# Optimization experiments

Hardware: AMD Instinct MI355X
Metric: run time of the kernel (lower is better)

Reference implementation:

```python
import jax, jax.numpy as jnp
import numpy as np

C = 256
BN_EPS = 1e-5


def conv1x1(x, w, b):
    # x: (B, Cin, H, W), w: (Cout, Cin), b: (Cout,)
    return jnp.einsum('bchw,oc->bohw', x, w) + b[None, :, None, None]


def setup_inputs() -> dict:
    key = jax.random.key(0)
    ks = jax.random.split(key, 12)
    B, H, W = 8, 64, 64
    s = 1.0 / np.sqrt(C)
    inp = {
        'xi': jax.random.normal(ks[0], (B, C, H, W), jnp.float32),
        'xj': jax.random.normal(ks[1], (B, C, H, W), jnp.float32),
        'g_w': jax.random.normal(ks[2], (C, C), jnp.float32) * s,
        'g_b': jax.random.normal(ks[3], (C,), jnp.float32) * s,
        'theta_w': jax.random.normal(ks[4], (C, C), jnp.float32) * s,
        'theta_b': jax.random.normal(ks[5], (C,), jnp.float32) * s,
        'phi_w': jax.random.normal(ks[6], (C, C), jnp.float32) * s,
        'phi_b': jax.random.normal(ks[7], (C,), jnp.float32) * s,
        'W_w': jax.random.normal(ks[8], (C, C), jnp.float32) * s,
        'W_b': jax.random.normal(ks[9], (C,), jnp.float32) * s,
        'bn_gamma': jnp.ones((C,), jnp.float32),
        'bn_beta': jnp.zeros((C,), jnp.float32),
    }
    return inp


def reference(xi, xj, g_w, g_b, theta_w, theta_b, phi_w, phi_b, W_w, W_b, bn_gamma, bn_beta):
    B, Cc, H, W = xi.shape
    N = H * W
    # 1x1 conv projections, flattened to token sequences
    g_x = conv1x1(xj, g_w, g_b).reshape(B, Cc, N)        # (B, C, N)
    theta_x = conv1x1(xi, theta_w, theta_b).reshape(B, Cc, N)  # (B, C, N)
    phi_x = conv1x1(xj, phi_w, phi_b).reshape(B, Cc, N)  # (B, C, N)
    # f = theta^T @ phi, scaled by N (no softmax)
    f = jnp.einsum('bcn,bcm->bnm', theta_x, phi_x) / N   # (B, N, N)
    # y = f @ g^T, back to channel-first
    y = jnp.einsum('bnm,bcm->bcn', f, g_x).reshape(B, Cc, H, W)
    W_y = conv1x1(y, W_w, W_b)
    z = W_y + xi
    # BatchNorm2d (training-mode batch statistics, biased variance)
    mean = jnp.mean(z, axis=(0, 2, 3), keepdims=True)
    var = jnp.var(z, axis=(0, 2, 3), keepdims=True)
    z_hat = (z - mean) * jax.lax.rsqrt(var + BN_EPS)
    return z_hat * bn_gamma[None, :, None, None] + bn_beta[None, :, None, None]
```

## Files before the change

### kernel.cpp

```cpp
#include <hip/hip_runtime.h>
#include <hip/hip_cooperative_groups.h>
#include <cstddef>

namespace cg = cooperative_groups;

#define CCH 256
#define NPIX 4096
#define NB 8
#define INVCNT (1.0f/32768.0f)
#define INVN (1.0f/4096.0f)

typedef __bf16 bf16_t;
typedef __attribute__((ext_vector_type(8))) __bf16 bf16x8;
typedef __attribute__((ext_vector_type(4))) __bf16 bf16x4;
typedef __attribute__((ext_vector_type(4))) float f32x4;

#define OFF_S      0u
#define OFF_AB     2048u
#define OFF_BMT    34816u
#define OFF_T1     67584u
#define OFF_R      67840u
#define OFF_W1     68096u
#define OFF_C1     68352u
#define OFF_G      68608u
#define OFF_MP     330752u
#define OFF_E      592896u
#define OFF_RSP    594944u
#define OFF_BSUM   627712u
#define OFF_BSQ    627968u
#define OFF_GP     890368u
#define OFF_XIT    5084672u

__device__ __forceinline__ void pack8(const float4& x, const float4& y, bf16x8& o) {
  o[0]=(bf16_t)x.x; o[1]=(bf16_t)x.y; o[2]=(bf16_t)x.z; o[3]=(bf16_t)x.w;
  o[4]=(bf16_t)y.x; o[5]=(bf16_t)y.y; o[6]=(bf16_t)y.z; o[7]=(bf16_t)y.w;
}

__device__ __forceinline__ void ld4(const float* p, float4& a0, float4& a1, float4& a2, float4& a3) {
  a0 = *(const float4*)p;       a1 = *(const float4*)(p + 4);
  a2 = *(const float4*)(p + 8); a3 = *(const float4*)(p + 12);
}

template <bool ATRANS>
__device__ __forceinline__ void mm64v(const float* __restrict__ A,
                                      const float* __restrict__ B,
                                      int i0, int j0,
                                      float (&acc)[2][4],
                                      float (*s1)[65], float (*s2)[65]) {
  const int t = threadIdx.x, tx = t & 15, ty = t >> 4;
  for (int k0 = 0; k0 < 256; k0 += 64) {
#pragma unroll
    for (int it = 0; it < 2; ++it) {
      const int f = t + 512 * it;
      const int row = f >> 4, cc = (f & 15) * 4;
      float4 va;
      if (ATRANS)
        va = *(const float4*)(A + (size_t)(k0 + row) * CCH + i0 + cc);
      else
        va = *(const float4*)(A + (size_t)(i0 + row) * CCH + k0 + cc);
      const float4 vb = *(const float4*)(B + (size_t)(k0 + row) * CCH + j0 + cc);
      s1[row][cc + 0] = va.x; s1[row][cc + 1] = va.y; s1[row][cc + 2] = va.z; s1[row][cc + 3] = va.w;
      s2[row][cc + 0] = vb.x; s2[row][cc + 1] = vb.y; s2[row][cc + 2] = vb.z; s2[row][cc + 3] = vb.w;
    }
    __syncthreads();
#pragma unroll 4
    for (int kk = 0; kk < 64; ++kk) {
      float ar[2], br[4];
#pragma unroll
      for (int i = 0; i < 2; ++i) ar[i] = ATRANS ? s1[kk][2 * ty + i] : s1[2 * ty + i][kk];
#pragma unroll
      for (int j = 0; j < 4; ++j) br[j] = s2[kk][4 * tx + j];
#pragma unroll
      for (int i = 0; i < 2; ++i)
#pragma unroll
        for (int j = 0; j < 4; ++j) acc[i][j] += ar[i] * br[j];
    }
    __syncthreads();
  }
}

__device__ void pre_body(int blk, const float* Ww, const float* gw, const float* phw,
                         const float* thw, const float* gb, const float* phb,
                         const float* thb, float* ws, unsigned char* SMEM) {
  const int t = threadIdx.x;
  if (blk < 32) {
    float (*s1)[65] = (float(*)[65])SMEM;
    float (*s2)[65] = (float(*)[65])(SMEM + 16640);
    const int tb = blk & 15;
    const int i0 = (tb >> 2) * 64, j0 = (tb & 3) * 64;
    float acc[2][4] = {};
    if (blk < 16) mm64v<false>(Ww, gw, i0, j0, acc, s1, s2);
    else          mm64v<true >(thw, phw, i0, j0, acc, s1, s2);
    bf16_t* outp = (bf16_t*)(ws + (blk < 16 ? OFF_AB : OFF_BMT));
    const int tx = t & 15, ty = t >> 4;
#pragma unroll
    for (int i = 0; i < 2; ++i) {
      bf16x4 mv;
#pragma unroll
      for (int q = 0; q < 4; ++q) mv[q] = (bf16_t)acc[i][q];
      *(bf16x4*)&outp[(size_t)(i0 + 2 * ty + i) * CCH + j0 + 4 * tx] = mv;
    }
  } else {
    if (t < 256) {
      float t1v = 0.f, rv = 0.f, w1v = 0.f;
      for (int k = 0; k < 256; ++k) {
        t1v += phw[k * CCH + t] * thb[k];
        rv  += thw[k * CCH + t] * phb[k];
        w1v += Ww[t * CCH + k] * gb[k];
      }
      ws[OFF_T1 + t] = t1v; ws[OFF_R + t] = rv; ws[OFF_W1 + t] = w1v;
    }
    float* red = (float*)SMEM;
    red[t] = (t < 256) ? phb[t] * thb[t] : 0.f;
    __syncthreads();
    for (int off = 256; off; off >>= 1) { if (t < off) red[t] += red[t + off]; __syncthreads(); }
    if (t == 0) ws[OFF_C1] = red[0];
  }
}

__device__ void cvtT_body(int bx, int b, const float* __restrict__ xi,
                          float* __restrict__ ws, unsigned char* SMEM) {
  bf16_t (*st)[72] = (bf16_t(*)[72])SMEM;
  const int c0 = (bx & 1) * 128;
  const int n0 = (bx >> 1) * 64;
  const float* X = xi + (size_t)b * CCH * NPIX;
  const int t = threadIdx.x;
  const int r = t >> 2, c4 = (t & 3) * 16;
  {
    float4 a0, a1, a2, a3;
    ld4(X + (size_t)(c0 + r) * NPIX + n0 + c4, a0, a1, a2, a3);
    bf16x8 u0, u1;
    pack8(a0, a1, u0); pack8(a2, a3, u1);
    *(bf16x8*)&st[r][c4] = u0;
    *(bf16x8*)&st[r][c4 + 8] = u1;
  }
  __syncthreads();
  bf16_t* Xit = (bf16_t*)(ws + OFF_XIT) + (size_t)b * NPIX * CCH;
  const int nr = t >> 3, cc = (t & 7) * 16;
  bf16x8 o0, o1;
#pragma unroll
  for (int j = 0; j < 8; ++j) o0[j] = st[cc + j][nr];
#pragma unroll
  for (int j = 0; j < 8; ++j) o1[j] = st[cc + 8 + j][nr];
  *(bf16x8*)(Xit + (size_t)(n0 + nr) * CCH + c0 + cc) = o0;
  *(bf16x8*)(Xit + (size_t)(n0 + nr) * CCH + c0 + cc + 8) = o1;
}

__device__ void gram_body(int ks, int b, const float* __restrict__ X,
                          float* __restrict__ ws, unsigned char* SMEM) {
  bf16_t (*sA)[256][40] = (bf16_t(*)[256][40])SMEM;
  const int t = threadIdx.x;
  const int w = t >> 6, lane = t & 63;
  const int wr = w >> 1, wc = w & 1;
  const int lr = lane & 15, hi = lane >> 4;
  const int fcol = 8 * hi;
  const f32x4 z4 = {0.f, 0.f, 0.f, 0.f};
  f32x4 acc[4][8];
#pragma unroll
  for (int fr = 0; fr < 4; ++fr)
#pragma unroll
    for (int fc = 0; fc < 8; ++fc) acc[fr][fc] = z4;
  float rsum = 0.f;
  const int k0 = ks * 256;
  const int srow = t >> 1, sh16 = (t & 1) * 16;

  float4 a0, a1, a2, a3;
  auto LOAD = [&](int kc) {
    ld4(X + (size_t)srow * NPIX + k0 + kc + sh16, a0, a1, a2, a3);
    rsum += a0.x + a0.y + a0.z + a0.w + a1.x + a1.y + a1.z + a1.w
          + a2.x + a2.y + a2.z + a2.w + a3.x + a3.y + a3.z + a3.w;
  };
  auto WRITE = [&](int q) {
    bf16x8 u0, u1;
    pack8(a0, a1, u0); pack8(a2, a3, u1);
    *(bf16x8*)&sA[q][srow][sh16] = u0;
    *(bf16x8*)&sA[q][srow][sh16 + 8] = u1;
  };

  LOAD(0);
  WRITE(0);
  __syncthreads();
  int cur = 0;
  for (int kc8 = 0; kc8 < 8; ++kc8) {
    if (kc8 < 7) LOAD(32 * (kc8 + 1));
    bf16x8 af[4];
#pragma unroll
    for (int fr = 0; fr < 4; ++fr)
      af[fr] = *(const bf16x8*)&sA[cur][64 * wr + 16 * fr + lr][fcol];
#pragma unroll
    for (int fc = 0; fc < 8; ++fc) {
      const bf16x8 bv = *(const bf16x8*)&sA[cur][128 * wc + 16 * fc + lr][fcol];
#pragma unroll
      for (int fr = 0; fr < 4; ++fr)
        acc[fr][fc] = __builtin_amdgcn_mfma_f32_16x16x32_bf16(af[fr], bv, acc[fr][fc], 0, 0, 0);
    }
    if (kc8 < 7) WRITE(cur ^ 1);
    __syncthreads();
    cur ^= 1;
  }

  {
    const float o = __shfl_down(rsum, 1);
    if (!(t & 1)) ws[OFF_RSP + ((size_t)(b * 16 + ks)) * CCH + srow] = rsum + o;
  }
  bf16_t* GPp = (bf16_t*)(ws + OFF_GP) + (size_t)(b * 16 + ks) * 65536;
  bf16_t (*sT)[264] = (bf16_t(*)[264])SMEM;
  const int rl = 16 * wr + 4 * hi;
#pragma unroll
  for (int fr = 0; fr < 4; ++fr) {
    __syncthreads();
#pragma unroll
    for (int fc = 0; fc < 8; ++fc)
#pragma unroll
      for (int reg = 0; reg < 4; ++reg)
        sT[rl + reg][128 * wc + 16 * fc + lr] = (bf16_t)acc[fr][fc][reg];
    __syncthreads();
    const int row = t >> 3;
    const int c32 = (t & 7) * 32;
    const int grow = 64 * (row >> 4) + 16 * fr + (row & 15);
#pragma unroll
    for (int q = 0; q < 4; ++q) {
      const bf16x8 v = *(const bf16x8*)&sT[row][c32 + 8 * q];
      *(bf16x8*)&GPp[(size_t)grow * CCH + c32 + 8 * q] = v;
    }
  }
}

__global__ __launch_bounds__(512) void k_mega(const float* __restrict__ xi,
                                              const float* __restrict__ xj,
                                              const float* __restrict__ Ww,
                                              const float* __restrict__ gw,
                                              const float* __restrict__ phw,
                                              const float* __restrict__ thw,
                                              const float* __restrict__ gb,
                                              const float* __restrict__ phb,
                                              const float* __restrict__ thb,
                                              float* __restrict__ ws) {
  __shared__ __align__(16) unsigned char SMEM[40960];
  const int bx = blockIdx.x, by = blockIdx.y;
  if (bx >= 144) {
    if (by == 0) pre_body(bx - 144, Ww, gw, phw, thw, gb, phb, thb, ws, SMEM);
    return;
  }
  if (bx >= 16) { cvtT_body(bx - 16, by, xi, ws, SMEM); return; }
  gram_body(bx, by, xj + (size_t)by * CCH * NPIX, ws, SMEM);
}

__global__ __launch_bounds__(256) void k_greduce(float* __restrict__ ws) {
  const int b = blockIdx.y, bx = blockIdx.x, t = threadIdx.x;
  const bf16_t* GPp = (const bf16_t*)(ws + OFF_GP) + (size_t)b * 16 * 65536;
  bf16_t* Gb = (bf16_t*)(ws + OFF_G) + (size_t)b * 65536;
  const int row = bx * 8 + (t >> 5);
  const int j8 = (t & 31) * 8;
  float s[8] = {};
#pragma unroll
  for (int ks = 0; ks < 16; ++ks) {
    const bf16x8 v = *(const bf16x8*)&GPp[(size_t)ks * 65536 + row * CCH + j8];
#pragma unroll
    for (int q = 0; q < 8; ++q) s[q] += (float)v[q];
  }
  bf16x8 o;
#pragma unroll
  for (int q = 0; q < 8; ++q) o[q] = (bf16_t)s[q];
  *(bf16x8*)&Gb[(size_t)row * CCH + j8] = o;
  if (t < 128) {
    const int rr = bx * 8 + (t >> 4), l = t & 15;
    float v = ws[OFF_RSP + ((size_t)(b * 16 + l)) * CCH + rr];
#pragma unroll
    for (int off = 8; off; off >>= 1) v += __shfl_down(v, off, 16);
    if (l == 0) ws[OFF_S + b * CCH + rr] = v;
  }
}

__global__ __launch_bounds__(256) void k_kmmat(const float* __restrict__ Wb, float* __restrict__ ws) {
  const int b = blockIdx.y;
  const int i0 = blockIdx.x * 32;
  const int t = threadIdx.x;
  const int w = t >> 6, lane = t & 63;
  const int rg = w >> 1, cw = w & 1;
  const int lr = lane & 15, hi = lane >> 4;
  const int fcol = 8 * hi;

  __shared__ __align__(16) bf16_t sA[2][32][40];
  __shared__ __align__(16) bf16_t sB[2][256][40];
  __shared__ __align__(16) bf16_t sK[32][264];
  __shared__ float sS[256], sT1[256], sR[256], sW1[256], sVS[256];
  __shared__ float sU[32];
  __shared__ float red[256];
  __shared__ float sdt_sh;

  const bf16_t* Ab  = (const bf16_t*)(ws + OFF_AB);
  const bf16_t* BmT = (const bf16_t*)(ws + OFF_BMT);
  const bf16_t* Gb  = (const bf16_t*)(ws + OFF_G) + (size_t)b * 65536;

  sS[t]  = ws[OFF_S + b * CCH + t];
  sT1[t] = ws[OFF_T1 + t];
  sR[t]  = ws[OFF_R + t];
  sW1[t] = ws[OFF_W1 + t];
  __syncthreads();
  red[t] = sS[t] * sT1[t];
  __syncthreads();
  for (int off = 128; off; off >>= 1) { if (t < off) red[t] += red[t + off]; __syncthreads(); }
  if (t == 0) sdt_sh = red[0];
  {
    float a = 0.f;
    for (int k8 = 0; k8 < 256; k8 += 8) {
      const bf16x8 v = *(const bf16x8*)&BmT[(size_t)t * CCH + k8];
#pragma unroll
      for (int q = 0; q < 8; ++q) a += (float)v[q] * sS[k8 + q];
    }
    sVS[t] = a;
  }
  if (t < 32) {
    float a = 0.f;
    for (int k8 = 0; k8 < 256; k8 += 8) {
      const bf16x8 v = *(const bf16x8*)&Ab[(size_t)(i0 + t) * CCH + k8];
#pragma unroll
      for (int q = 0; q < 8; ++q) a += (float)v[q] * sS[k8 + q];
    }
    sU[t] = a;
  }

  const f32x4 z4 = {0.f, 0.f, 0.f, 0.f};
  const int arow = t >> 2, achk = (t & 3) * 8;

  f32x4 acc[8];
#pragma unroll
  for (int fc = 0; fc < 8; ++fc) acc[fc] = z4;
  bf16x8 ra;
  bf16x8 gb8[4];
  auto LOADB = [&](int k) {
    if (t < 128) ra = *(const bf16x8*)&Ab[(size_t)(i0 + arow) * CCH + k + achk];
#pragma unroll
    for (int h = 0; h < 4; ++h)
      gb8[h] = *(const bf16x8*)&Gb[(size_t)(64 * h + arow) * CCH + k + achk];
  };
  auto WRITEB = [&](int q) {
    if (t < 128) *(bf16x8*)&sA[q][arow][achk] = ra;
#pragma unroll
    for (int h = 0; h < 4; ++h)
      *(bf16x8*)&sB[q][64 * h + arow][achk] = gb8[h];
  };
  LOADB(0);
  WRITEB(0);
  __syncthreads();
  int cur = 0;
  for (int ks = 0; ks < 8; ++ks) {
    if (ks < 7) LOADB(32 * (ks + 1));
    const bf16x8 af = *(const bf16x8*)&sA[cur][16 * rg + lr][fcol];
#pragma unroll
    for (int fc = 0; fc < 8; ++fc) {
      const bf16x8 bv = *(const bf16x8*)&sB[cur][128 * cw + 16 * fc + lr][fcol];
      acc[fc] = __builtin_amdgcn_mfma_f32_16x16x32_bf16(af, bv, acc[fc], 0, 0, 0);
    }
    if (ks < 7) WRITEB(cur ^ 1);
    __syncthreads();
    cur ^= 1;
  }
#pragma unroll
  for (int fc = 0; fc < 8; ++fc)
#pragma unroll
    for (int reg = 0; reg < 4; ++reg)
      sK[16 * rg + 4 * hi + reg][128 * cw + 16 * fc + lr] = (bf16_t)acc[fc][reg];
  __syncthreads();

  if (t < 32) {
    float dot = 0.f;
    for (int k8 = 0; k8 < 256; k8 += 8) {
      const bf16x8 v = *(const bf16x8*)&sK[t][k8];
#pragma unroll
      for (int q = 0; q < 8; ++q) dot += (float)v[q] * sT1[k8 + q];
    }
    const float c1 = ws[OFF_C1];
    const float ui = sU[t], w1i = sW1[i0 + t];
    ws[OFF_E + b * CCH + i0 + t] = INVN * (dot + c1 * ui + sdt_sh * w1i) + c1 * w1i + Wb[i0 + t];
  }

  f32x4 acc2[8];
#pragma unroll
  for (int fc = 0; fc < 8; ++fc) acc2[fc] = z4;
  bf16x8 rb[4];
  auto LOADC = [&](int k) {
#pragma unroll
    for (int h = 0; h < 4; ++h)
      rb[h] = *(const bf16x8*)&BmT[(size_t)(64 * h + arow) * CCH + k + achk];
  };
  auto WRITEC = [&](int q) {
#pragma unroll
    for (int h = 0; h < 4; ++h)
      *(bf16x8*)&sB[q][64 * h + arow][achk] = rb[h];
  };
  LOADC(0);
  WRITEC(0);
  __syncthreads();
  cur = 0;
  for (int ks = 0; ks < 8; ++ks) {
    if (ks < 7) LOADC(32 * (ks + 1));
    const bf16x8 af = *(const bf16x8*)&sK[16 * rg + lr][32 * ks + fcol];
#pragma unroll
    for (int fc = 0; fc < 8; ++fc) {
      const bf16x8 bv = *(const bf16x8*)&sB[cur][128 * cw + 16 * fc + lr][fcol];
      acc2[fc] = __builtin_amdgcn_mfma_f32_16x16x32_bf16(af, bv, acc2[fc], 0, 0, 0);
    }
    if (ks < 7) WRITEC(cur ^ 1);
    __syncthreads();
    cur ^= 1;
  }

  bf16_t* Mp = (bf16_t*)(ws + OFF_MP) + (size_t)b * 65536;
#pragma unroll
  for (int fc = 0; fc < 8; ++fc) {
    const int j = 128 * cw + 16 * fc + lr;
    const float rj = sR[j], vsj = sVS[j];
#pragma unroll
    for (int reg = 0; reg < 4; ++reg) {
      const int il = 16 * rg + 4 * hi + reg;
      const float ui = sU[il], w1i = sW1[i0 + il];
      float m = (acc2[fc][reg] + ui * rj + w1i * vsj) * INVN + w1i * rj;
      if (i0 + il == j) m += 1.0f;
      sK[16 * rg + 4 * hi + reg][128 * cw + 16 * fc + lr] = (bf16_t)m;
    }
  }
  __syncthreads();
  {
    const int row = t >> 3;
    const int c32 = (t & 7) * 32;
#pragma unroll
    for (int q = 0; q < 4; ++q) {
      const bf16x8 v = *(const bf16x8*)&sK[row][c32 + 8 * q];
      *(bf16x8*)&Mp[(size_t)(i0 + row) * CCH + c32 + 8 * q] = v;
    }
  }
}

__device__ __forceinline__ void zmm_core(const float* __restrict__ ws, int b, int n0,
                                         f32x4 (&acc)[2][8],
                                         bf16_t (*sA)[64][40], bf16_t (*sB)[256][40]) {
  const int t = threadIdx.x;
  const int lane = t & 63;
  const int w = t >> 6;
  const int rg = w >> 1, cw = w & 1;
  const int lr = lane & 15, hi = lane >> 4;
  const bf16_t* Xit = (const bf16_t*)(ws + OFF_XIT) + (size_t)b * NPIX * CCH;
  const bf16_t* Mp = (const bf16_t*)(ws + OFF_MP) + (size_t)b * 65536;
  const int arow = t >> 2, achk = (t & 3) * 8;
  bf16x8 ra, rb0, rb1, rb2, rb3;
  ra  = *(const bf16x8*)(Xit + (size_t)(n0 + arow) * CCH + achk);
  rb0 = *(const bf16x8*)(Mp + (size_t)(arow)       * CCH + achk);
  rb1 = *(const bf16x8*)(Mp + (size_t)(64 + arow)  * CCH + achk);
  rb2 = *(const bf16x8*)(Mp + (size_t)(128 + arow) * CCH + achk);
  rb3 = *(const bf16x8*)(Mp + (size_t)(192 + arow) * CCH + achk);
  *(bf16x8*)&sA[0][arow][achk] = ra;
  *(bf16x8*)&sB[0][arow][achk] = rb0;
  *(bf16x8*)&sB[0][64 + arow][achk] = rb1;
  *(bf16x8*)&sB[0][128 + arow][achk] = rb2;
  *(bf16x8*)&sB[0][192 + arow][achk] = rb3;
  __syncthreads();
  int cur = 0;
  for (int ks = 0; ks < 8; ++ks) {
    const int nk = 32 * (ks + 1);
    if (ks < 7) {
      ra  = *(const bf16x8*)(Xit + (size_t)(n0 + arow) * CCH + nk + achk);
      rb0 = *(const bf16x8*)(Mp + (size_t)(arow)       * CCH + nk + achk);
      rb1 = *(const bf16x8*)(Mp + (size_t)(64 + arow)  * CCH + nk + achk);
      rb2 = *(const bf16x8*)(Mp + (size_t)(128 + arow) * CCH + nk + achk);
      rb3 = *(const bf16x8*)(Mp + (size_t)(192 + arow) * CCH + nk + achk);
    }
    const int fcol = 8 * hi;
    const bf16x8 af0 = *(const bf16x8*)&sA[cur][32 * rg + lr][fcol];
    const bf16x8 af1 = *(const bf16x8*)&sA[cur][32 * rg + 16 + lr][fcol];
#pragma unroll
    for (int fc = 0; fc < 8; ++fc) {
      const bf16x8 bv = *(const bf16x8*)&sB[cur][128 * cw + 16 * fc + lr][fcol];
      acc[0][fc] = __builtin_amdgcn_mfma_f32_16x16x32_bf16(af0, bv, acc[0][fc], 0, 0, 0);
      acc[1][fc] = __builtin_amdgcn_mfma_f32_16x16x32_bf16(af1, bv, acc[1][fc], 0, 0, 0);
    }
    if (ks < 7) {
      *(bf16x8*)&sA[cur ^ 1][arow][achk] = ra;
      *(bf16x8*)&sB[cur ^ 1][arow][achk] = rb0;
      *(bf16x8*)&sB[cur ^ 1][64 + arow][achk] = rb1;
      *(bf16x8*)&sB[cur ^ 1][128 + arow][achk] = rb2;
      *(bf16x8*)&sB[cur ^ 1][192 + arow][achk] = rb3;
    }
    __syncthreads();
    cur ^= 1;
  }
}

__device__ __forceinline__ void bn_partials_atomic(float* __restrict__ ws, const float* sE,
                                                   f32x4 (&acc)[2][8],
                                                   float (*redS)[128], float (*redQ)[128]) {
  const int t = threadIdx.x;
  const int lane = t & 63, w = t >> 6;
  const int cw = w & 1, lr = lane & 15;
  float ps[8], pq[8];
#pragma unroll
  for (int fc = 0; fc < 8; ++fc) {
    const int c = 128 * cw + 16 * fc + lr;
    const float e = sE[c];
    float s = 0.f, q = 0.f;
#pragma unroll
    for (int fr = 0; fr < 2; ++fr)
#pragma unroll
      for (int reg = 0; reg < 4; ++reg) {
        const float z = acc[fr][fc][reg] + e;
        s += z; q += z * z;
      }
    s += __shfl_xor(s, 16); s += __shfl_xor(s, 32);
    q += __shfl_xor(q, 16); q += __shfl_xor(q, 32);
    ps[fc] = s; pq[fc] = q;
  }
  if (lane < 16) {
#pragma unroll
    for (int fc = 0; fc < 8; ++fc) {
      redS[w][16 * fc + lane] = ps[fc];
      redQ[w][16 * fc + lane] = pq[fc];
    }
  }
  __syncthreads();
  {
    const int cg2 = t >> 7, c = t & 127;
    float s = 0.f, q = 0.f;
#pragma unroll
    for (int rg2 = 0; rg2 < 2; ++rg2) {
      s += redS[rg2 * 2 + cg2][c];
      q += redQ[rg2 * 2 + cg2][c];
    }
    atomicAdd(&ws[OFF_BSUM + t], s);
    atomicAdd(&ws[OFF_BSQ + t], q);
  }
}

__device__ __forceinline__ void z_apply(const float* sC1, const float* sC2,
                                        f32x4 (&acc)[2][8],
                                        float* __restrict__ out, int b, int n0) {
  const int t = threadIdx.x;
  const int lane = t & 63, w = t >> 6;
  const int rg = w >> 1, cw = w & 1;
  const int lr = lane & 15, hi = lane >> 4;
#pragma unroll
  for (int fc = 0; fc < 8; ++fc) {
    const int c = 128 * cw + 16 * fc + lr;
    const float sc = sC1[c], b2 = sC2[c];
    float* op = out + ((size_t)b * CCH + c) * NPIX + n0 + 32 * rg + 4 * hi;
#pragma unroll
    for (int fr = 0; fr < 2; ++fr) {
      float4 v;
      v.x = acc[fr][fc][0] * sc + b2;
      v.y = acc[fr][fc][1] * sc + b2;
      v.z = acc[fr][fc][2] * sc + b2;
      v.w = acc[fr][fc][3] * sc + b2;
      *(float4*)(op + 16 * fr) = v;
    }
  }
}

__global__ __launch_bounds__(256) void k_zstat(float* __restrict__ ws) {
  const int b = blockIdx.y, n0 = blockIdx.x * 64;
  const int t = threadIdx.x;
  __shared__ __align__(16) bf16_t sA[2][64][40];
  __shared__ __align__(16) bf16_t sB[2][256][40];
  __shared__ float sE[256];
  __shared__ float redS[4][128], redQ[4][128];
  sE[t] = ws[OFF_E + b * CCH + t];
  const f32x4 z4 = {0.f, 0.f, 0.f, 0.f};
  f32x4 acc[2][8];
#pragma unroll
  for (int fr = 0; fr < 2; ++fr)
#pragma unroll
    for (int fc = 0; fc < 8; ++fc) acc[fr][fc] = z4;
  zmm_core(ws, b, n0, acc, sA, sB);
  bn_partials_atomic(ws, sE, acc, redS, redQ);
}

__global__ __launch_bounds__(256) void k_zapply(float* __restrict__ ws, float* __restrict__ out,
                                                const float* __restrict__ gamma,
                                                const float* __restrict__ beta) {
  const int b = blockIdx.y, n0 = blockIdx.x * 64;
  const int t = threadIdx.x;
  __shared__ __align__(16) bf16_t sA[2][64][40];
  __shared__ __align__(16) bf16_t sB[2][256][40];
  __shared__ float sC1[256], sC2[256];
  {
    const float e = ws[OFF_E + b * CCH + t];
    const float sv = ws[OFF_BSUM + t], qv = ws[OFF_BSQ + t];
    const float mean = sv * INVCNT;
    const float var = qv * INVCNT - mean * mean;
    const float sc = gamma[t] * rsqrtf(var + 1e-5f);
    sC1[t] = sc;
    sC2[t] = e * sc + beta[t] - mean * sc;
  }
  const f32x4 z4 = {0.f, 0.f, 0.f, 0.f};
  f32x4 acc[2][8];
#pragma unroll
  for (int fr = 0; fr < 2; ++fr)
#pragma unroll
    for (int fc = 0; fc < 8; ++fc) acc[fr][fc] = z4;
  zmm_core(ws, b, n0, acc, sA, sB);
  z_apply(sC1, sC2, acc, out, b, n0);
}

__global__ __launch_bounds__(256, 2) void k_zfused(float* __restrict__ ws,
                                                   float* __restrict__ out,
                                                   const float* __restrict__ gamma,
                                                   const float* __restrict__ beta) {
  const int bid = blockIdx.x;
  const int b = bid >> 6, n0 = (bid & 63) * 64;
  const int t = threadIdx.x;
  __shared__ __align__(16) bf16_t sA[2][64][40];
  __shared__ __align__(16) bf16_t sB[2][256][40];
  __shared__ float sE[256];
  __shared__ float sC1[256], sC2[256];
  __shared__ float redS[4][128], redQ[4][128];
  sE[t] = ws[OFF_E + b * CCH + t];
  const f32x4 z4 = {0.f, 0.f, 0.f, 0.f};
  f32x4 acc[2][8];
#pragma unroll
  for (int fr = 0; fr < 2; ++fr)
#pragma unroll
    for (int fc = 0; fc < 8; ++fc) acc[fr][fc] = z4;
  zmm_core(ws, b, n0, acc, sA, sB);
  bn_partials_atomic(ws, sE, acc, redS, redQ);
  cg::this_grid().sync();
  {
    const float sv = ws[OFF_BSUM + t], qv = ws[OFF_BSQ + t];
    const float mean = sv * INVCNT;
    const float var = qv * INVCNT - mean * mean;
    const float sc = gamma[t] * rsqrtf(var + 1e-5f);
    sC1[t] = sc;
    sC2[t] = sE[t] * sc + beta[t] - mean * sc;
  }
  __syncthreads();
  z_apply(sC1, sC2, acc, out, b, n0);
}

extern "C" void kernel_launch(void* const* d_in, const int* in_sizes, int n_in,
                              void* d_out, int out_size, void* d_ws, size_t ws_size,
                              hipStream_t stream) {
  const float* xi  = (const float*)d_in[0];
  const float* xj  = (const float*)d_in[1];
  const float* gw  = (const float*)d_in[2];
  const float* gb  = (const float*)d_in[3];
  const float* thw = (const float*)d_in[4];
  const float* thb = (const float*)d_in[5];
  const float* phw = (const float*)d_in[6];
  const float* phb = (const float*)d_in[7];
  const float* Ww  = (const float*)d_in[8];
  const float* Wb  = (const float*)d_in[9];
  const float* gamma = (const float*)d_in[10];
  const float* beta  = (const float*)d_in[11];
  float* ws = (float*)d_ws;
  float* out = (float*)d_out;

  k_mega<<<dim3(177, 8), 512, 0, stream>>>(xi, xj, Ww, gw, phw, thw, gb, phb, thb, ws);
  k_greduce<<<dim3(32, 8), 256, 0, stream>>>(ws);
  k_kmmat<<<dim3(8, 8), 256, 0, stream>>>(Wb, ws);
  hipMemsetAsync(ws + OFF_BSUM, 0, 512 * sizeof(float), stream);

  int dev = 0;
  hipGetDevice(&dev);
  int coopAttr = 0;
  hipDeviceGetAttribute(&coopAttr, hipDeviceAttributeCooperativeLaunch, dev);
  int maxb = 0;
  if (coopAttr)
    hipOccupancyMaxActiveBlocksPerMultiprocessor(&maxb, k_zfused, 256, 0);

  bool done = false;
  if (coopAttr && maxb >= 2) {
    float* wsp = ws;
    float* outp = out;
    const float* gammap = gamma;
    const float* betap = beta;
    void* args[] = {(void*)&wsp, (void*)&outp, (void*)&gammap, (void*)&betap};
    hipError_t err = hipLaunchCooperativeKernel((void*)k_zfused, dim3(512), dim3(256),
                                                args, 0, stream);
    done = (err == hipSuccess);
  }
  if (!done) {
    k_zstat<<<dim3(64, 8), 256, 0, stream>>>(ws);
    k_zapply<<<dim3(64, 8), 256, 0, stream>>>(ws, out, gamma, beta);
  }
}
```

Baseline: 96.30 us.

## Drop cooperative grid-sync kernel; recompute z GEMM in separate stat and apply kernels

Removes the cooperative-launch fused kernel that held accumulators across a grid-wide sync. It always runs two kernels instead, one computing BN partial sums and one recomputing the GEMM and applying normalization. It also moves zeroing of the BN accumulators into k_kmmat, replacing a hipMemsetAsync. This avoids the grid-sync, the host-side attribute and occupancy queries, and the memset launch, at the cost of running the z GEMM twice.

```diff
diff --git a/kernel.cpp b/kernel.cpp
--- a/kernel.cpp
+++ b/kernel.cpp
@@ -1,8 +1,5 @@
 #include <hip/hip_runtime.h>
-#include <hip/hip_cooperative_groups.h>
 #include <cstddef>
-
-namespace cg = cooperative_groups;
 
 #define CCH 256
 #define NPIX 4096
@@ -280,6 +277,11 @@
   const int rg = w >> 1, cw = w & 1;
   const int lr = lane & 15, hi = lane >> 4;
   const int fcol = 8 * hi;
+
+  if (blockIdx.x == 0 && b == 0) {
+    ws[OFF_BSUM + t] = 0.f;
+    ws[OFF_BSQ + t] = 0.f;
+  }
 
   __shared__ __align__(16) bf16_t sA[2][32][40];
   __shared__ __align__(16) bf16_t sB[2][256][40];
@@ -487,12 +489,23 @@
   }
 }
 
-__device__ __forceinline__ void bn_partials_atomic(float* __restrict__ ws, const float* sE,
-                                                   f32x4 (&acc)[2][8],
-                                                   float (*redS)[128], float (*redQ)[128]) {
+__global__ __launch_bounds__(256) void k_zstat(float* __restrict__ ws) {
+  const int b = blockIdx.y, n0 = blockIdx.x * 64;
   const int t = threadIdx.x;
   const int lane = t & 63, w = t >> 6;
   const int cw = w & 1, lr = lane & 15;
+  __shared__ __align__(16) bf16_t sA[2][64][40];
+  __shared__ __align__(16) bf16_t sB[2][256][40];
+  __shared__ float sE[256];
+  __shared__ float redS[4][128], redQ[4][128];
+  sE[t] = ws[OFF_E + b * CCH + t];
+  const f32x4 z4 = {0.f, 0.f, 0.f, 0.f};
+  f32x4 acc[2][8];
+#pragma unroll
+  for (int fr = 0; fr < 2; ++fr)
+#pragma unroll
+    for (int fc = 0; fc < 8; ++fc) acc[fr][fc] = z4;
+  zmm_core(ws, b, n0, acc, sA, sB);
   float ps[8], pq[8];
 #pragma unroll
   for (int fc = 0; fc < 8; ++fc) {
@@ -531,53 +544,14 @@
   }
 }
 
-__device__ __forceinline__ void z_apply(const float* sC1, const float* sC2,
-                                        f32x4 (&acc)[2][8],
-                                        float* __restrict__ out, int b, int n0) {
-  const int t = threadIdx.x;
-  const int lane = t & 63, w = t >> 6;
-  const int rg = w >> 1, cw = w & 1;
-  const int lr = lane & 15, hi = lane >> 4;
-#pragma unroll
-  for (int fc = 0; fc < 8; ++fc) {
-    const int c = 128 * cw + 16 * fc + lr;
-    const float sc = sC1[c], b2 = sC2[c];
-    float* op = out + ((size_t)b * CCH + c) * NPIX + n0 + 32 * rg + 4 * hi;
-#pragma unroll
-    for (int fr = 0; fr < 2; ++fr) {
-      float4 v;
-      v.x = acc[fr][fc][0] * sc + b2;
-      v.y = acc[fr][fc][1] * sc + b2;
-      v.z = acc[fr][fc][2] * sc + b2;
-      v.w = acc[fr][fc][3] * sc + b2;
-      *(float4*)(op + 16 * fr) = v;
-    }
-  }
-}
-
-__global__ __launch_bounds__(256) void k_zstat(float* __restrict__ ws) {
-  const int b = blockIdx.y, n0 = blockIdx.x * 64;
-  const int t = threadIdx.x;
-  __shared__ __align__(16) bf16_t sA[2][64][40];
-  __shared__ __align__(16) bf16_t sB[2][256][40];
-  __shared__ float sE[256];
-  __shared__ float redS[4][128], redQ[4][128];
-  sE[t] = ws[OFF_E + b * CCH + t];
-  const f32x4 z4 = {0.f, 0.f, 0.f, 0.f};
-  f32x4 acc[2][8];
-#pragma unroll
-  for (int fr = 0; fr < 2; ++fr)
-#pragma unroll
-    for (int fc = 0; fc < 8; ++fc) acc[fr][fc] = z4;
-  zmm_core(ws, b, n0, acc, sA, sB);
-  bn_partials_atomic(ws, sE, acc, redS, redQ);
-}
-
 __global__ __launch_bounds__(256) void k_zapply(float* __restrict__ ws, float* __restrict__ out,
                                                 const float* __restrict__ gamma,
                                                 const float* __restrict__ beta) {
   const int b = blockIdx.y, n0 = blockIdx.x * 64;
   const int t = threadIdx.x;
+  const int lane = t & 63, w = t >> 6;
+  const int rg = w >> 1, cw = w & 1;
+  const int lr = lane & 15, hi = lane >> 4;
   __shared__ __align__(16) bf16_t sA[2][64][40];
   __shared__ __align__(16) bf16_t sB[2][256][40];
   __shared__ float sC1[256], sC2[256];
@@ -597,41 +571,21 @@
 #pragma unroll
     for (int fc = 0; fc < 8; ++fc) acc[fr][fc] = z4;
   zmm_core(ws, b, n0, acc, sA, sB);
-  z_apply(sC1, sC2, acc, out, b, n0);
-}
-
-__global__ __launch_bounds__(256, 2) void k_zfused(float* __restrict__ ws,
-                                                   float* __restrict__ out,
-                                                   const float* __restrict__ gamma,
-                                                   const float* __restrict__ beta) {
-  const int bid = blockIdx.x;
-  const int b = bid >> 6, n0 = (bid & 63) * 64;
-  const int t = threadIdx.x;
-  __shared__ __align__(16) bf16_t sA[2][64][40];
-  __shared__ __align__(16) bf16_t sB[2][256][40];
-  __shared__ float sE[256];
-  __shared__ float sC1[256], sC2[256];
-  __shared__ float redS[4][128], redQ[4][128];
-  sE[t] = ws[OFF_E + b * CCH + t];
-  const f32x4 z4 = {0.f, 0.f, 0.f, 0.f};
-  f32x4 acc[2][8];
-#pragma unroll
-  for (int fr = 0; fr < 2; ++fr)
-#pragma unroll
-    for (int fc = 0; fc < 8; ++fc) acc[fr][fc] = z4;
-  zmm_core(ws, b, n0, acc, sA, sB);
-  bn_partials_atomic(ws, sE, acc, redS, redQ);
-  cg::this_grid().sync();
-  {
-    const float sv = ws[OFF_BSUM + t], qv = ws[OFF_BSQ + t];
-    const float mean = sv * INVCNT;
-    const float var = qv * INVCNT - mean * mean;
-    const float sc = gamma[t] * rsqrtf(var + 1e-5f);
-    sC1[t] = sc;
-    sC2[t] = sE[t] * sc + beta[t] - mean * sc;
-  }
-  __syncthreads();
-  z_apply(sC1, sC2, acc, out, b, n0);
+#pragma unroll
+  for (int fc = 0; fc < 8; ++fc) {
+    const int c = 128 * cw + 16 * fc + lr;
+    const float sc = sC1[c], b2 = sC2[c];
+    float* op = out + ((size_t)b * CCH + c) * NPIX + n0 + 32 * rg + 4 * hi;
+#pragma unroll
+    for (int fr = 0; fr < 2; ++fr) {
+      float4 v;
+      v.x = acc[fr][fc][0] * sc + b2;
+      v.y = acc[fr][fc][1] * sc + b2;
+      v.z = acc[fr][fc][2] * sc + b2;
+      v.w = acc[fr][fc][3] * sc + b2;
+      *(float4*)(op + 16 * fr) = v;
+    }
+  }
 }
 
 extern "C" void kernel_launch(void* const* d_in, const int* in_sizes, int n_in,
@@ -655,29 +609,6 @@
   k_mega<<<dim3(177, 8), 512, 0, stream>>>(xi, xj, Ww, gw, phw, thw, gb, phb, thb, ws);
   k_greduce<<<dim3(32, 8), 256, 0, stream>>>(ws);
   k_kmmat<<<dim3(8, 8), 256, 0, stream>>>(Wb, ws);
-  hipMemsetAsync(ws + OFF_BSUM, 0, 512 * sizeof(float), stream);
-
-  int dev = 0;
-  hipGetDevice(&dev);
-  int coopAttr = 0;
-  hipDeviceGetAttribute(&coopAttr, hipDeviceAttributeCooperativeLaunch, dev);
-  int maxb = 0;
-  if (coopAttr)
-    hipOccupancyMaxActiveBlocksPerMultiprocessor(&maxb, k_zfused, 256, 0);
-
-  bool done = false;
-  if (coopAttr && maxb >= 2) {
-    float* wsp = ws;
-    float* outp = out;
-    const float* gammap = gamma;
-    const float* betap = beta;
-    void* args[] = {(void*)&wsp, (void*)&outp, (void*)&gammap, (void*)&betap};
-    hipError_t err = hipLaunchCooperativeKernel((void*)k_zfused, dim3(512), dim3(256),
-                                                args, 0, stream);
-    done = (err == hipSuccess);
-  }
-  if (!done) {
-    k_zstat<<<dim3(64, 8), 256, 0, stream>>>(ws);
-    k_zapply<<<dim3(64, 8), 256, 0, stream>>>(ws, out, gamma, beta);
-  }
-}
+  k_zstat<<<dim3(64, 8), 256, 0, stream>>>(ws);
+  k_zapply<<<dim3(64, 8), 256, 0, stream>>>(ws, out, gamma, beta);
+}
```

Measured after the change: 94.96 us. About the same (-1.4%).
